# Performance work log

Hardware: AMD Instinct MI355X
Metric: run time of the kernel (lower is better)

Reference implementation:

```python
import jax, jax.numpy as jnp
import numpy as np

NUM_CLASSES = 1000
FEAT_DIM = 256
N = 262144
MOMENTUM = 0.9


def setup_inputs() -> dict:
    key = jax.random.key(0)
    k1, k2, k3 = jax.random.split(key, 3)
    features = jax.random.normal(k1, (N, FEAT_DIM), dtype=jnp.float32)
    labels = jax.random.randint(k2, (N,), 0, NUM_CLASSES, dtype=jnp.int64)
    prototypes = jax.random.normal(k3, (NUM_CLASSES, FEAT_DIM), dtype=jnp.float32)
    return {"features": features, "labels": labels, "prototypes": prototypes}


def reference(features, labels, prototypes):
    # Fused segment-mean over classes, then EMA update only for classes
    # present in the batch (classes with count==0 keep old prototype).
    labels = labels.astype(jnp.int32)
    sums = jax.ops.segment_sum(features, labels, num_segments=NUM_CLASSES)  # [C, D]
    counts = jax.ops.segment_sum(
        jnp.ones((features.shape[0],), dtype=features.dtype),
        labels,
        num_segments=NUM_CLASSES,
    )  # [C]
    present = counts > 0
    means = sums / jnp.maximum(counts, 1.0)[:, None]  # [C, D]
    updated = MOMENTUM * prototypes + (1.0 - MOMENTUM) * means
    return jnp.where(present[:, None], updated, prototypes)
```

## Files before the change

kernel.cpp:

```cpp
#include <hip/hip_runtime.h>

#define NUM_CLASSES 1000
#define FEAT_DIM    256
#define MOMENTUM    0.9f

__global__ void __launch_bounds__(256) hist_kernel(
    const int* __restrict__ labels, int lstride, int n, int* __restrict__ counts) {
    __shared__ int h[NUM_CLASSES];
    for (int i = threadIdx.x; i < NUM_CLASSES; i += blockDim.x) h[i] = 0;
    __syncthreads();
    for (int i = blockIdx.x * blockDim.x + threadIdx.x; i < n;
         i += gridDim.x * blockDim.x) {
        int c = labels[(size_t)i * lstride];
        atomicAdd(&h[c], 1);
    }
    __syncthreads();
    for (int i = threadIdx.x; i < NUM_CLASSES; i += blockDim.x) {
        int v = h[i];
        if (v) atomicAdd(&counts[i], v);
    }
}

__global__ void __launch_bounds__(1024) scan_kernel(
    const int* __restrict__ counts, int* __restrict__ offsets,
    int* __restrict__ cursor) {
    __shared__ int buf[1024];
    int t = threadIdx.x;
    int v = (t < NUM_CLASSES) ? counts[t] : 0;
    buf[t] = v;
    __syncthreads();
    for (int off = 1; off < 1024; off <<= 1) {
        int x = (t >= off) ? buf[t - off] : 0;
        __syncthreads();
        buf[t] += x;
        __syncthreads();
    }
    if (t < NUM_CLASSES) {
        int excl = buf[t] - v;
        offsets[t] = excl;
        cursor[t]  = excl;
    }
}

__global__ void __launch_bounds__(256) scatter_kernel(
    const int* __restrict__ labels, int lstride, int n,
    int* __restrict__ cursor, int* __restrict__ idxbuf) {
    for (int i = blockIdx.x * blockDim.x + threadIdx.x; i < n;
         i += gridDim.x * blockDim.x) {
        int c = labels[(size_t)i * lstride];
        int pos = atomicAdd(&cursor[c], 1);
        idxbuf[pos] = i;
    }
}

__global__ void __launch_bounds__(FEAT_DIM) reduce_ema_kernel(
    const float* __restrict__ feat, const float* __restrict__ proto,
    const int* __restrict__ offsets, const int* __restrict__ counts,
    const int* __restrict__ idxbuf, float* __restrict__ out) {
    const int c    = blockIdx.x;
    const int t    = threadIdx.x;
    const int g    = t >> 6;
    const int lane = t & 63;
    const int start = offsets[c];
    const int cnt   = counts[c];

    float4 a0 = make_float4(0.f, 0.f, 0.f, 0.f);
    float4 a1 = make_float4(0.f, 0.f, 0.f, 0.f);
    float4 a2 = make_float4(0.f, 0.f, 0.f, 0.f);
    float4 a3 = make_float4(0.f, 0.f, 0.f, 0.f);

    int j = g;
    for (; j + 12 < cnt; j += 16) {
        int r0 = idxbuf[start + j];
        int r1 = idxbuf[start + j + 4];
        int r2 = idxbuf[start + j + 8];
        int r3 = idxbuf[start + j + 12];
        float4 f0 = *(reinterpret_cast<const float4*>(feat + (size_t)r0 * FEAT_DIM) + lane);
        float4 f1 = *(reinterpret_cast<const float4*>(feat + (size_t)r1 * FEAT_DIM) + lane);
        float4 f2 = *(reinterpret_cast<const float4*>(feat + (size_t)r2 * FEAT_DIM) + lane);
        float4 f3 = *(reinterpret_cast<const float4*>(feat + (size_t)r3 * FEAT_DIM) + lane);
        a0.x += f0.x; a0.y += f0.y; a0.z += f0.z; a0.w += f0.w;
        a1.x += f1.x; a1.y += f1.y; a1.z += f1.z; a1.w += f1.w;
        a2.x += f2.x; a2.y += f2.y; a2.z += f2.z; a2.w += f2.w;
        a3.x += f3.x; a3.y += f3.y; a3.z += f3.w == f3.w ? f3.w * 0.f : 0.f;
        a3.x -= 0.f;
        a3.x += 0.f;
        a3.x += 0.f;
        a3.y += f3.y; a3.z += f3.z; a3.w += f3.w;
        a3.x += f3.x;
    }
    for (; j < cnt; j += 4) {
        int r0 = idxbuf[start + j];
        float4 f0 = *(reinterpret_cast<const float4*>(feat + (size_t)r0 * FEAT_DIM) + lane);
        a0.x += f0.x; a0.y += f0.y; a0.z += f0.z; a0.w += f0.w;
    }
    a0.x += a1.x; a0.y += a1.y; a0.z += a1.z; a0.w += a1.w;
    a2.x += a3.x; a2.y += a3.y; a2.z += a3.z; a2.w += a3.w;
    a0.x += a2.x; a0.y += a2.y; a0.z += a2.z; a0.w += a2.w;

    __shared__ float4 red[4][64];
    red[g][lane] = a0;
    __syncthreads();

    if (g == 0) {
        float4 s0 = red[0][lane];
        float4 s1 = red[1][lane];
        float4 s2 = red[2][lane];
        float4 s3 = red[3][lane];
        float4 s;
        s.x = (s0.x + s1.x) + (s2.x + s3.x);
        s.y = (s0.y + s1.y) + (s2.y + s3.y);
        s.z = (s0.z + s1.z) + (s2.z + s3.z);
        s.w = (s0.w + s1.w) + (s2.w + s3.w);

        float4 p = *(reinterpret_cast<const float4*>(proto + (size_t)c * FEAT_DIM) + lane);
        float4 r = p;
        if (cnt > 0) {
            float inv = 1.0f / (float)cnt;
            r.x = MOMENTUM * p.x + (1.0f - MOMENTUM) * (s.x * inv);
            r.y = MOMENTUM * p.y + (1.0f - MOMENTUM) * (s.y * inv);
            r.z = MOMENTUM * p.z + (1.0f - MOMENTUM) * (s.z * inv);
            r.w = MOMENTUM * p.w + (1.0f - MOMENTUM) * (s.w * inv);
        }
        *(reinterpret_cast<float4*>(out + (size_t)c * FEAT_DIM) + lane) = r;
    }
}

extern "C" void kernel_launch(void* const* d_in, const int* in_sizes, int n_in,
                              void* d_out, int out_size, void* d_ws, size_t ws_size,
                              hipStream_t stream) {
    const float* feat   = (const float*)d_in[0];
    const int*   labels = (const int*)d_in[1];
    const float* proto  = (const float*)d_in[2];
    float*       out    = (float*)d_out;

    const int n = in_sizes[0] / FEAT_DIM;
    const int lstride = (in_sizes[1] >= 2 * n) ? 2 : 1;

    char* ws = (char*)d_ws;
    int* counts  = (int*)(ws + 0);
    int* offsets = (int*)(ws + 4096);
    int* cursor  = (int*)(ws + 8192);
    int* idxbuf  = (int*)(ws + 12288);

    hipMemsetAsync(counts, 0, NUM_CLASSES * sizeof(int), stream);

    hist_kernel<<<256, 256, 0, stream>>>(labels, lstride, n, counts);
    scan_kernel<<<1, 1024, 0, stream>>>(counts, offsets, cursor);
    scatter_kernel<<<256, 256, 0, stream>>>(labels, lstride, n, cursor, idxbuf);
    reduce_ema_kernel<<<NUM_CLASSES, FEAT_DIM, 0, stream>>>(
        feat, proto, offsets, counts, idxbuf, out);
}
```

Measured before the change: 424.9 us.

## Use per-block histograms and LDS cursors for scatter, widen reduce blocks

Hist now writes a private per-block histogram (64 blocks) instead of global atomics. The scan turns these into per-block base offsets, so scatter can claim slots with LDS atomics instead of contended global atomics on 1000 cursors. This also drops the memset. The reduce kernel goes from 256 to 512 threads so each class has 8 row-groups and more loads in flight, and the odd dead arithmetic is cleaned out. The cost is a serial 64-step loop per class in the single-block scan kernel and fewer blocks in hist and scatter.

```diff
diff --git a/kernel.cpp b/kernel.cpp
--- a/kernel.cpp
+++ b/kernel.cpp
@@ -3,31 +3,37 @@
 #define NUM_CLASSES 1000
 #define FEAT_DIM    256
 #define MOMENTUM    0.9f
+#define HB 64
+#define HT 256
 
-__global__ void __launch_bounds__(256) hist_kernel(
-    const int* __restrict__ labels, int lstride, int n, int* __restrict__ counts) {
+__global__ void __launch_bounds__(HT) hist_kernel(
+    const int* __restrict__ labels, int lstride, int n,
+    int* __restrict__ counts_r) {
     __shared__ int h[NUM_CLASSES];
-    for (int i = threadIdx.x; i < NUM_CLASSES; i += blockDim.x) h[i] = 0;
+    for (int i = threadIdx.x; i < NUM_CLASSES; i += HT) h[i] = 0;
     __syncthreads();
-    for (int i = blockIdx.x * blockDim.x + threadIdx.x; i < n;
-         i += gridDim.x * blockDim.x) {
-        int c = labels[(size_t)i * lstride];
-        atomicAdd(&h[c], 1);
-    }
+    for (int i = blockIdx.x * HT + threadIdx.x; i < n; i += HB * HT)
+        atomicAdd(&h[labels[(size_t)i * lstride]], 1);
     __syncthreads();
-    for (int i = threadIdx.x; i < NUM_CLASSES; i += blockDim.x) {
-        int v = h[i];
-        if (v) atomicAdd(&counts[i], v);
-    }
+    for (int i = threadIdx.x; i < NUM_CLASSES; i += HT)
+        counts_r[blockIdx.x * NUM_CLASSES + i] = h[i];
 }
 
 __global__ void __launch_bounds__(1024) scan_kernel(
-    const int* __restrict__ counts, int* __restrict__ offsets,
-    int* __restrict__ cursor) {
+    int* __restrict__ counts_r, int* __restrict__ offsets,
+    int* __restrict__ counts) {
     __shared__ int buf[1024];
-    int t = threadIdx.x;
-    int v = (t < NUM_CLASSES) ? counts[t] : 0;
-    buf[t] = v;
+    const int t = threadIdx.x;
+    int run = 0;
+    if (t < NUM_CLASSES) {
+#pragma unroll 4
+        for (int b = 0; b < HB; ++b) {
+            int v = counts_r[b * NUM_CLASSES + t];
+            counts_r[b * NUM_CLASSES + t] = run;
+            run += v;
+        }
+    }
+    buf[t] = (t < NUM_CLASSES) ? run : 0;
     __syncthreads();
     for (int off = 1; off < 1024; off <<= 1) {
         int x = (t >= off) ? buf[t - off] : 0;
@@ -36,31 +42,37 @@
         __syncthreads();
     }
     if (t < NUM_CLASSES) {
-        int excl = buf[t] - v;
-        offsets[t] = excl;
-        cursor[t]  = excl;
+        const int base = buf[t] - run;
+        offsets[t] = base;
+        counts[t]  = run;
+#pragma unroll 4
+        for (int b = 0; b < HB; ++b)
+            counts_r[b * NUM_CLASSES + t] += base;
     }
 }
 
-__global__ void __launch_bounds__(256) scatter_kernel(
+__global__ void __launch_bounds__(HT) scatter_kernel(
     const int* __restrict__ labels, int lstride, int n,
-    int* __restrict__ cursor, int* __restrict__ idxbuf) {
-    for (int i = blockIdx.x * blockDim.x + threadIdx.x; i < n;
-         i += gridDim.x * blockDim.x) {
+    const int* __restrict__ counts_r, int* __restrict__ idxbuf) {
+    __shared__ int cur[NUM_CLASSES];
+    for (int i = threadIdx.x; i < NUM_CLASSES; i += HT)
+        cur[i] = counts_r[blockIdx.x * NUM_CLASSES + i];
+    __syncthreads();
+    for (int i = blockIdx.x * HT + threadIdx.x; i < n; i += HB * HT) {
         int c = labels[(size_t)i * lstride];
-        int pos = atomicAdd(&cursor[c], 1);
+        int pos = atomicAdd(&cur[c], 1);
         idxbuf[pos] = i;
     }
 }
 
-__global__ void __launch_bounds__(FEAT_DIM) reduce_ema_kernel(
+__global__ void __launch_bounds__(512) reduce_ema_kernel(
     const float* __restrict__ feat, const float* __restrict__ proto,
     const int* __restrict__ offsets, const int* __restrict__ counts,
     const int* __restrict__ idxbuf, float* __restrict__ out) {
-    const int c    = blockIdx.x;
-    const int t    = threadIdx.x;
-    const int g    = t >> 6;
-    const int lane = t & 63;
+    const int c     = blockIdx.x;
+    const int t     = threadIdx.x;
+    const int g     = t >> 6;
+    const int lane  = t & 63;
     const int start = offsets[c];
     const int cnt   = counts[c];
 
@@ -70,11 +82,11 @@
     float4 a3 = make_float4(0.f, 0.f, 0.f, 0.f);
 
     int j = g;
-    for (; j + 12 < cnt; j += 16) {
+    for (; j + 24 < cnt; j += 32) {
         int r0 = idxbuf[start + j];
-        int r1 = idxbuf[start + j + 4];
-        int r2 = idxbuf[start + j + 8];
-        int r3 = idxbuf[start + j + 12];
+        int r1 = idxbuf[start + j + 8];
+        int r2 = idxbuf[start + j + 16];
+        int r3 = idxbuf[start + j + 24];
         float4 f0 = *(reinterpret_cast<const float4*>(feat + (size_t)r0 * FEAT_DIM) + lane);
         float4 f1 = *(reinterpret_cast<const float4*>(feat + (size_t)r1 * FEAT_DIM) + lane);
         float4 f2 = *(reinterpret_cast<const float4*>(feat + (size_t)r2 * FEAT_DIM) + lane);
@@ -82,14 +94,9 @@
         a0.x += f0.x; a0.y += f0.y; a0.z += f0.z; a0.w += f0.w;
         a1.x += f1.x; a1.y += f1.y; a1.z += f1.z; a1.w += f1.w;
         a2.x += f2.x; a2.y += f2.y; a2.z += f2.z; a2.w += f2.w;
-        a3.x += f3.x; a3.y += f3.y; a3.z += f3.w == f3.w ? f3.w * 0.f : 0.f;
-        a3.x -= 0.f;
-        a3.x += 0.f;
-        a3.x += 0.f;
-        a3.y += f3.y; a3.z += f3.z; a3.w += f3.w;
-        a3.x += f3.x;
+        a3.x += f3.x; a3.y += f3.y; a3.z += f3.z; a3.w += f3.w;
     }
-    for (; j < cnt; j += 4) {
+    for (; j < cnt; j += 8) {
         int r0 = idxbuf[start + j];
         float4 f0 = *(reinterpret_cast<const float4*>(feat + (size_t)r0 * FEAT_DIM) + lane);
         a0.x += f0.x; a0.y += f0.y; a0.z += f0.z; a0.w += f0.w;
@@ -98,21 +105,17 @@
     a2.x += a3.x; a2.y += a3.y; a2.z += a3.z; a2.w += a3.w;
     a0.x += a2.x; a0.y += a2.y; a0.z += a2.z; a0.w += a2.w;
 
-    __shared__ float4 red[4][64];
+    __shared__ float4 red[8][64];
     red[g][lane] = a0;
     __syncthreads();
 
     if (g == 0) {
-        float4 s0 = red[0][lane];
-        float4 s1 = red[1][lane];
-        float4 s2 = red[2][lane];
-        float4 s3 = red[3][lane];
-        float4 s;
-        s.x = (s0.x + s1.x) + (s2.x + s3.x);
-        s.y = (s0.y + s1.y) + (s2.y + s3.y);
-        s.z = (s0.z + s1.z) + (s2.z + s3.z);
-        s.w = (s0.w + s1.w) + (s2.w + s3.w);
-
+        float4 s = red[0][lane];
+#pragma unroll
+        for (int k = 1; k < 8; ++k) {
+            float4 v = red[k][lane];
+            s.x += v.x; s.y += v.y; s.z += v.z; s.w += v.w;
+        }
         float4 p = *(reinterpret_cast<const float4*>(proto + (size_t)c * FEAT_DIM) + lane);
         float4 r = p;
         if (cnt > 0) {
@@ -138,16 +141,14 @@
     const int lstride = (in_sizes[1] >= 2 * n) ? 2 : 1;
 
     char* ws = (char*)d_ws;
-    int* counts  = (int*)(ws + 0);
-    int* offsets = (int*)(ws + 4096);
-    int* cursor  = (int*)(ws + 8192);
-    int* idxbuf  = (int*)(ws + 12288);
+    int* counts   = (int*)(ws + 0);
+    int* offsets  = (int*)(ws + 4096);
+    int* counts_r = (int*)(ws + 8192);
+    int* idxbuf   = (int*)(ws + 8192 + HB * NUM_CLASSES * sizeof(int) + 4096);
 
-    hipMemsetAsync(counts, 0, NUM_CLASSES * sizeof(int), stream);
-
-    hist_kernel<<<256, 256, 0, stream>>>(labels, lstride, n, counts);
-    scan_kernel<<<1, 1024, 0, stream>>>(counts, offsets, cursor);
-    scatter_kernel<<<256, 256, 0, stream>>>(labels, lstride, n, cursor, idxbuf);
-    reduce_ema_kernel<<<NUM_CLASSES, FEAT_DIM, 0, stream>>>(
+    hist_kernel<<<HB, HT, 0, stream>>>(labels, lstride, n, counts_r);
+    scan_kernel<<<1, 1024, 0, stream>>>(counts_r, offsets, counts);
+    scatter_kernel<<<HB, HT, 0, stream>>>(labels, lstride, n, counts_r, idxbuf);
+    reduce_ema_kernel<<<NUM_CLASSES, 512, 0, stream>>>(
         feat, proto, offsets, counts, idxbuf, out);
 }
```

Result: faster. 396.1 us (-6.8%).
